# Kernel optimization log

Measured on AMD Instinct MI355X. Metric: run time of the kernel, lower is better.

## Reference

```python
import jax, jax.numpy as jnp
import numpy as np

B = 16384

def setup_inputs() -> dict:
    key = jax.random.key(0)
    ks = jax.random.split(key, 10)
    def lin(kw, fan_in, fan_out):
        lim = 1.0 / np.sqrt(fan_in)
        k1, k2 = jax.random.split(kw)
        w = jax.random.uniform(k1, (fan_out, fan_in), jnp.float32, -lim, lim)
        b = jax.random.uniform(k2, (fan_out,), jnp.float32, -lim, lim)
        return w, b
    x = jax.random.normal(ks[0], (B, 784), dtype=jnp.float32)
    conv_w = jnp.ones((3, 3), dtype=jnp.float32)
    w1, b1 = lin(ks[1], 676, 256)
    w2, b2 = lin(ks[2], 256, 128)
    w3, b3 = lin(ks[3], 128, 64)
    w4, b4 = lin(ks[4], 64, 10)
    return {"x": x, "conv_w": conv_w, "w1": w1, "b1": b1, "w2": w2, "b2": b2,
            "w3": w3, "b3": b3, "w4": w4, "b4": b4}

def reference(x, conv_w, w1, b1, w2, b2, w3, b3, w4, b4):
    b = x.shape[0]
    img = x.reshape(b, 1, 28, 28)                      # NCHW
    kern = conv_w.reshape(1, 1, 3, 3)                   # OIHW
    conv = jax.lax.conv_general_dilated(
        img, kern, window_strides=(1, 1), padding='VALID',
        dimension_numbers=('NCHW', 'OIHW', 'NCHW'))     # [B,1,26,26]
    h = conv.reshape(b, 26 * 26)
    h1 = jax.nn.relu(h @ w1.T + b1)
    h2 = jax.nn.relu(h1 @ w2.T + b2)
    h3 = jax.nn.relu(h2 @ w3.T + b3)
    out = h3 @ w4.T + b4                                # [B,10] logits
    return out
```

## Files before the change

kernel.cpp:

```cpp
#include <hip/hip_runtime.h>
#include <hip/hip_bf16.h>

typedef __attribute__((ext_vector_type(8))) short bf16x8;
typedef __attribute__((ext_vector_type(4))) float f32x4;

__device__ __forceinline__ unsigned short f2bf(float f) {
  unsigned int u = __builtin_bit_cast(unsigned int, f);
  u += 0x7fffu + ((u >> 16) & 1u);
  return (unsigned short)(u >> 16);
}

__device__ __forceinline__ f32x4 mfma16(bf16x8 a, bf16x8 b, f32x4 c) {
  return __builtin_amdgcn_mfma_f32_16x16x32_bf16(a, b, c, 0, 0, 0);
}

__global__ void prep_weights(const float* __restrict__ w1, const float* __restrict__ w2,
                             const float* __restrict__ w3, const float* __restrict__ w4,
                             unsigned short* __restrict__ w1b, unsigned short* __restrict__ w2b,
                             unsigned short* __restrict__ w3b, unsigned short* __restrict__ w4b) {
  const int idx = blockIdx.x * blockDim.x + threadIdx.x;
  const int stride = gridDim.x * blockDim.x;
  for (int i = idx; i < 256 * 704; i += stride) {
    int o = i / 704, k = i - o * 704;
    w1b[i] = f2bf(k < 676 ? w1[o * 676 + k] : 0.f);
  }
  for (int i = idx; i < 128 * 256; i += stride) w2b[i] = f2bf(w2[i]);
  for (int i = idx; i < 64 * 128; i += stride) w3b[i] = f2bf(w3[i]);
  for (int i = idx; i < 16 * 64; i += stride) {
    int o = i >> 6, k = i & 63;
    w4b[i] = f2bf(o < 10 ? w4[o * 64 + k] : 0.f);
  }
}

#define LDS_TOTAL 145408

__global__ __launch_bounds__(512, 2) void fused_mlp(
    const float* __restrict__ x,
    const float* __restrict__ cw,
    const unsigned short* __restrict__ w1b,
    const unsigned short* __restrict__ w2b,
    const unsigned short* __restrict__ w3b,
    const unsigned short* __restrict__ w4b,
    const float* __restrict__ b1, const float* __restrict__ b2,
    const float* __restrict__ b3, const float* __restrict__ b4,
    float* __restrict__ out)
{
  extern __shared__ char lds[];
  unsigned short* hbT = (unsigned short*)(lds);
  unsigned short* w1s = (unsigned short*)(lds + 91136);
  unsigned short* h1s = (unsigned short*)(lds + 111616);
  unsigned short* w2s = (unsigned short*)(lds);
  unsigned short* h2s = (unsigned short*)(lds + 91136);
  unsigned short* w3s = (unsigned short*)(lds + 111616);
  unsigned short* h3s = (unsigned short*)(lds);
  unsigned short* w4s = (unsigned short*)(lds + 91136);

  const int tid = threadIdx.x;
  const int lane = tid & 63;
  const int lane15 = lane & 15;
  const int kg = (lane >> 4) << 3;
  const int w = tid >> 6;
  const int wr = w >> 2;
  const int wc = w & 3;
  const int row0 = blockIdx.x * 64;

  {
    const float c0 = cw[0], c1 = cw[1], c2 = cw[2];
    const float c3 = cw[3], c4 = cw[4], c5 = cw[5];
    const float c6 = cw[6], c7 = cw[7], c8 = cw[8];
    const float* xblk = x + (size_t)row0 * 784;
    for (int f = tid; f < 64 * 182; f += 512) {
      int rr = f / 182;
      int t = f - rr * 182;
      int i = t / 7;
      int jq = t - i * 7;
      int j0 = jq << 2;
      const float* xr = xblk + rr * 784 + i * 28 + j0;
      if (jq < 6) {
        float4 v00 = *(const float4*)(xr);
        float4 v01 = *(const float4*)(xr + 4);
        float4 v10 = *(const float4*)(xr + 28);
        float4 v11 = *(const float4*)(xr + 32);
        float4 v20 = *(const float4*)(xr + 56);
        float4 v21 = *(const float4*)(xr + 60);
        float r0[8] = {v00.x, v00.y, v00.z, v00.w, v01.x, v01.y, v01.z, v01.w};
        float r1[8] = {v10.x, v10.y, v10.z, v10.w, v11.x, v11.y, v11.z, v11.w};
        float r2[8] = {v20.x, v20.y, v20.z, v20.w, v21.x, v21.y, v21.z, v21.w};
        float o[4];
#pragma unroll
        for (int tt = 0; tt < 4; ++tt) {
          o[tt] = c0 * r0[tt] + c1 * r0[tt + 1] + c2 * r0[tt + 2]
                + c3 * r1[tt] + c4 * r1[tt + 1] + c5 * r1[tt + 2]
                + c6 * r2[tt] + c7 * r2[tt + 1] + c8 * r2[tt + 2];
        }
        unsigned int p0 = (unsigned)f2bf(o[0]) | ((unsigned)f2bf(o[1]) << 16);
        unsigned int p1 = (unsigned)f2bf(o[2]) | ((unsigned)f2bf(o[3]) << 16);
        unsigned int* dst = (unsigned int*)(hbT + rr * 712 + i * 26 + j0);
        dst[0] = p0;
        dst[1] = p1;
      } else {
        float4 v0 = *(const float4*)(xr);
        float4 v1 = *(const float4*)(xr + 28);
        float4 v2 = *(const float4*)(xr + 56);
        float o0 = c0 * v0.x + c1 * v0.y + c2 * v0.z
                 + c3 * v1.x + c4 * v1.y + c5 * v1.z
                 + c6 * v2.x + c7 * v2.y + c8 * v2.z;
        float o1 = c0 * v0.y + c1 * v0.z + c2 * v0.w
                 + c3 * v1.y + c4 * v1.z + c5 * v1.w
                 + c6 * v2.y + c7 * v2.z + c8 * v2.w;
        unsigned int p0 = (unsigned)f2bf(o0) | ((unsigned)f2bf(o1) << 16);
        *(unsigned int*)(hbT + rr * 712 + i * 26 + 24) = p0;
      }
    }
    for (int f = tid; f < 64 * 14; f += 512) {
      int rr = f / 14, u = f - rr * 14;
      *(unsigned int*)(hbT + rr * 712 + 676 + (u << 1)) = 0u;
    }
  }

  f32x4 acc1[2][4] = {};
  __syncthreads();

  for (int ks = 0; ks < 22; ++ks) {
    const int k0 = ks << 5;
    {
      int f = tid;
#pragma unroll
      for (int it = 0; it < 2; ++it, f += 512) {
        int o = f >> 2, part = f & 3;
        *(uint4*)(w1s + o * 40 + (part << 3)) =
            *(const uint4*)(w1b + o * 704 + k0 + (part << 3));
      }
    }
    __syncthreads();
    bf16x8 a0 = *(const bf16x8*)(hbT + (wr * 32 + lane15) * 712 + k0 + kg);
    bf16x8 a1 = *(const bf16x8*)(hbT + (wr * 32 + 16 + lane15) * 712 + k0 + kg);
    bf16x8 fb0 = *(const bf16x8*)(w1s + (wc * 64 + lane15) * 40 + kg);
    bf16x8 fb1 = *(const bf16x8*)(w1s + (wc * 64 + 16 + lane15) * 40 + kg);
    bf16x8 fb2 = *(const bf16x8*)(w1s + (wc * 64 + 32 + lane15) * 40 + kg);
    bf16x8 fb3 = *(const bf16x8*)(w1s + (wc * 64 + 48 + lane15) * 40 + kg);
    acc1[0][0] = mfma16(a0, fb0, acc1[0][0]);
    acc1[0][1] = mfma16(a0, fb1, acc1[0][1]);
    acc1[0][2] = mfma16(a0, fb2, acc1[0][2]);
    acc1[0][3] = mfma16(a0, fb3, acc1[0][3]);
    acc1[1][0] = mfma16(a1, fb0, acc1[1][0]);
    acc1[1][1] = mfma16(a1, fb1, acc1[1][1]);
    acc1[1][2] = mfma16(a1, fb2, acc1[1][2]);
    acc1[1][3] = mfma16(a1, fb3, acc1[1][3]);
    __syncthreads();
  }

  {
    const int rb = wr * 32 + ((lane >> 4) << 2);
    const int cb = wc * 64 + lane15;
#pragma unroll
    for (int n = 0; n < 4; ++n) {
      const int col = cb + n * 16;
      const float bias = b1[col];
#pragma unroll
      for (int m = 0; m < 2; ++m) {
#pragma unroll
        for (int r = 0; r < 4; ++r) {
          float v = acc1[m][n][r] + bias;
          v = v > 0.f ? v : 0.f;
          h1s[(rb + m * 16 + r) * 264 + col] = f2bf(v);
        }
      }
    }
  }
  {
    int f = tid;
#pragma unroll
    for (int it = 0; it < 8; ++it, f += 512) {
      int o = f >> 5, part = f & 31;
      *(uint4*)(w2s + o * 264 + (part << 3)) =
          *(const uint4*)(w2b + o * 256 + (part << 3));
    }
  }
  __syncthreads();

  f32x4 acc2[2][2] = {};
  {
    const int ar = wr * 32 + lane15;
    const int bc = wc * 32 + lane15;
#pragma unroll
    for (int ks = 0; ks < 8; ++ks) {
      const int k0 = ks << 5;
      bf16x8 a0 = *(const bf16x8*)(h1s + ar * 264 + k0 + kg);
      bf16x8 a1 = *(const bf16x8*)(h1s + (ar + 16) * 264 + k0 + kg);
      bf16x8 fb0 = *(const bf16x8*)(w2s + bc * 264 + k0 + kg);
      bf16x8 fb1 = *(const bf16x8*)(w2s + (bc + 16) * 264 + k0 + kg);
      acc2[0][0] = mfma16(a0, fb0, acc2[0][0]);
      acc2[0][1] = mfma16(a0, fb1, acc2[0][1]);
      acc2[1][0] = mfma16(a1, fb0, acc2[1][0]);
      acc2[1][1] = mfma16(a1, fb1, acc2[1][1]);
    }
  }
  {
    const int rb = wr * 32 + ((lane >> 4) << 2);
    const int cb2 = wc * 32 + lane15;
#pragma unroll
    for (int n = 0; n < 2; ++n) {
      const int col = cb2 + n * 16;
      const float bias = b2[col];
#pragma unroll
      for (int m = 0; m < 2; ++m) {
#pragma unroll
        for (int r = 0; r < 4; ++r) {
          float v = acc2[m][n][r] + bias;
          v = v > 0.f ? v : 0.f;
          h2s[(rb + m * 16 + r) * 136 + col] = f2bf(v);
        }
      }
    }
  }
  __syncthreads();
  {
    int f = tid;
#pragma unroll
    for (int it = 0; it < 2; ++it, f += 512) {
      int o = f >> 4, part = f & 15;
      *(uint4*)(w3s + o * 136 + (part << 3)) =
          *(const uint4*)(w3b + o * 128 + (part << 3));
    }
  }
  __syncthreads();

  f32x4 acc3[2] = {};
  {
    const int ar = wr * 32 + lane15;
    const int bc3 = wc * 16 + lane15;
#pragma unroll
    for (int ks = 0; ks < 4; ++ks) {
      const int k0 = ks << 5;
      bf16x8 a0 = *(const bf16x8*)(h2s + ar * 136 + k0 + kg);
      bf16x8 a1 = *(const bf16x8*)(h2s + (ar + 16) * 136 + k0 + kg);
      bf16x8 fb0 = *(const bf16x8*)(w3s + bc3 * 136 + k0 + kg);
      acc3[0] = mfma16(a0, fb0, acc3[0]);
      acc3[1] = mfma16(a1, fb0, acc3[1]);
    }
    const int rb = wr * 32 + ((lane >> 4) << 2);
    const int col = bc3;
    const float bias = b3[col];
#pragma unroll
    for (int m = 0; m < 2; ++m) {
#pragma unroll
      for (int r = 0; r < 4; ++r) {
        float v = acc3[m][r] + bias;
        v = v > 0.f ? v : 0.f;
        h3s[(rb + m * 16 + r) * 72 + col] = f2bf(v);
      }
    }
  }
  __syncthreads();
  if (tid < 128) {
    int o = tid >> 3, part = tid & 7;
    *(uint4*)(w4s + o * 72 + (part << 3)) =
        *(const uint4*)(w4b + o * 64 + (part << 3));
  }
  __syncthreads();

  if (w < 4) {
    f32x4 acc4 = {};
    const int ar4 = w * 16 + lane15;
#pragma unroll
    for (int ks = 0; ks < 2; ++ks) {
      const int k0 = ks << 5;
      bf16x8 a0 = *(const bf16x8*)(h3s + ar4 * 72 + k0 + kg);
      bf16x8 fb0 = *(const bf16x8*)(w4s + lane15 * 72 + k0 + kg);
      acc4 = mfma16(a0, fb0, acc4);
    }
    const int col = lane15;
    if (col < 10) {
      const float bias = b4[col];
      const int rb4 = w * 16 + ((lane >> 4) << 2);
#pragma unroll
      for (int r = 0; r < 4; ++r) {
        out[(row0 + rb4 + r) * 10 + col] = acc4[r] + bias;
      }
    }
  }
}

extern "C" void kernel_launch(void* const* d_in, const int* in_sizes, int n_in,
                              void* d_out, int out_size, void* d_ws, size_t ws_size,
                              hipStream_t stream) {
  const float* x  = (const float*)d_in[0];
  const float* cw = (const float*)d_in[1];
  const float* w1 = (const float*)d_in[2];
  const float* b1 = (const float*)d_in[3];
  const float* w2 = (const float*)d_in[4];
  const float* b2 = (const float*)d_in[5];
  const float* w3 = (const float*)d_in[6];
  const float* b3 = (const float*)d_in[7];
  const float* w4 = (const float*)d_in[8];
  const float* b4 = (const float*)d_in[9];
  float* out = (float*)d_out;

  unsigned short* w1b = (unsigned short*)d_ws;
  unsigned short* w2b = w1b + 256 * 704;
  unsigned short* w3b = w2b + 128 * 256;
  unsigned short* w4b = w3b + 64 * 128;

  hipLaunchKernelGGL(prep_weights, dim3(128), dim3(256), 0, stream,
                     w1, w2, w3, w4, w1b, w2b, w3b, w4b);

  hipFuncSetAttribute((const void*)fused_mlp,
                      hipFuncAttributeMaxDynamicSharedMemorySize, LDS_TOTAL);
  hipLaunchKernelGGL(fused_mlp, dim3(256), dim3(512), LDS_TOTAL, stream,
                     x, cw, w1b, w2b, w3b, w4b, b1, b2, b3, b4, out);
}
```

Baseline: 134.6 us.

## Read weights directly from global memory and halve rows per block

Weight fragments are now loaded straight from global/L2 into MFMA operands instead of being staged through LDS with two barriers per K step. The block shrinks to 32 rows and 256 threads, with 512 blocks and about 45KB of static LDS instead of 145KB dynamic, so more blocks can fit per CU. Each wave now covers all 32 rows and a 64-column slice of layer 1. Every block rereads the full weight matrices from cache and the weight loads are uncoalesced strided row reads, which could raise L2 traffic.

New measurement: 140.3 us. 4.2% more time.

```diff
diff --git a/kernel.cpp b/kernel.cpp
--- a/kernel.cpp
+++ b/kernel.cpp
@@ -32,9 +32,7 @@
   }
 }
 
-#define LDS_TOTAL 145408
-
-__global__ __launch_bounds__(512, 2) void fused_mlp(
+__global__ __launch_bounds__(256, 2) void fused_mlp(
     const float* __restrict__ x,
     const float* __restrict__ cw,
     const unsigned short* __restrict__ w1b,
@@ -45,31 +43,26 @@
     const float* __restrict__ b3, const float* __restrict__ b4,
     float* __restrict__ out)
 {
-  extern __shared__ char lds[];
-  unsigned short* hbT = (unsigned short*)(lds);
-  unsigned short* w1s = (unsigned short*)(lds + 91136);
-  unsigned short* h1s = (unsigned short*)(lds + 111616);
-  unsigned short* w2s = (unsigned short*)(lds);
-  unsigned short* h2s = (unsigned short*)(lds + 91136);
-  unsigned short* w3s = (unsigned short*)(lds + 111616);
-  unsigned short* h3s = (unsigned short*)(lds);
-  unsigned short* w4s = (unsigned short*)(lds + 91136);
+  __shared__ unsigned short lds_s[22784];
+  unsigned short* hbT = lds_s;
+  unsigned short* h1s = lds_s;
+  unsigned short* h2s = lds_s + 8448;
+  unsigned short* h3s = lds_s + 12800;
 
   const int tid = threadIdx.x;
   const int lane = tid & 63;
   const int lane15 = lane & 15;
   const int kg = (lane >> 4) << 3;
   const int w = tid >> 6;
-  const int wr = w >> 2;
-  const int wc = w & 3;
-  const int row0 = blockIdx.x * 64;
+  const int row0 = blockIdx.x * 32;
+  const int rb = (lane >> 4) << 2;
 
   {
     const float c0 = cw[0], c1 = cw[1], c2 = cw[2];
     const float c3 = cw[3], c4 = cw[4], c5 = cw[5];
     const float c6 = cw[6], c7 = cw[7], c8 = cw[8];
     const float* xblk = x + (size_t)row0 * 784;
-    for (int f = tid; f < 64 * 182; f += 512) {
+    for (int f = tid; f < 32 * 182; f += 256) {
       int rr = f / 182;
       int t = f - rr * 182;
       int i = t / 7;
@@ -112,135 +105,108 @@
         *(unsigned int*)(hbT + rr * 712 + i * 26 + 24) = p0;
       }
     }
-    for (int f = tid; f < 64 * 14; f += 512) {
+    for (int f = tid; f < 32 * 14; f += 256) {
       int rr = f / 14, u = f - rr * 14;
       *(unsigned int*)(hbT + rr * 712 + 676 + (u << 1)) = 0u;
     }
   }
 
+  __syncthreads();
+
   f32x4 acc1[2][4] = {};
-  __syncthreads();
-
-  for (int ks = 0; ks < 22; ++ks) {
-    const int k0 = ks << 5;
-    {
-      int f = tid;
-#pragma unroll
-      for (int it = 0; it < 2; ++it, f += 512) {
-        int o = f >> 2, part = f & 3;
-        *(uint4*)(w1s + o * 40 + (part << 3)) =
-            *(const uint4*)(w1b + o * 704 + k0 + (part << 3));
-      }
-    }
-    __syncthreads();
-    bf16x8 a0 = *(const bf16x8*)(hbT + (wr * 32 + lane15) * 712 + k0 + kg);
-    bf16x8 a1 = *(const bf16x8*)(hbT + (wr * 32 + 16 + lane15) * 712 + k0 + kg);
-    bf16x8 fb0 = *(const bf16x8*)(w1s + (wc * 64 + lane15) * 40 + kg);
-    bf16x8 fb1 = *(const bf16x8*)(w1s + (wc * 64 + 16 + lane15) * 40 + kg);
-    bf16x8 fb2 = *(const bf16x8*)(w1s + (wc * 64 + 32 + lane15) * 40 + kg);
-    bf16x8 fb3 = *(const bf16x8*)(w1s + (wc * 64 + 48 + lane15) * 40 + kg);
-    acc1[0][0] = mfma16(a0, fb0, acc1[0][0]);
-    acc1[0][1] = mfma16(a0, fb1, acc1[0][1]);
-    acc1[0][2] = mfma16(a0, fb2, acc1[0][2]);
-    acc1[0][3] = mfma16(a0, fb3, acc1[0][3]);
-    acc1[1][0] = mfma16(a1, fb0, acc1[1][0]);
-    acc1[1][1] = mfma16(a1, fb1, acc1[1][1]);
-    acc1[1][2] = mfma16(a1, fb2, acc1[1][2]);
-    acc1[1][3] = mfma16(a1, fb3, acc1[1][3]);
-    __syncthreads();
-  }
-
-  {
-    const int rb = wr * 32 + ((lane >> 4) << 2);
-    const int cb = wc * 64 + lane15;
-#pragma unroll
-    for (int n = 0; n < 4; ++n) {
-      const int col = cb + n * 16;
-      const float bias = b1[col];
-#pragma unroll
-      for (int m = 0; m < 2; ++m) {
-#pragma unroll
-        for (int r = 0; r < 4; ++r) {
-          float v = acc1[m][n][r] + bias;
-          v = v > 0.f ? v : 0.f;
-          h1s[(rb + m * 16 + r) * 264 + col] = f2bf(v);
-        }
-      }
-    }
-  }
-  {
-    int f = tid;
-#pragma unroll
-    for (int it = 0; it < 8; ++it, f += 512) {
-      int o = f >> 5, part = f & 31;
-      *(uint4*)(w2s + o * 264 + (part << 3)) =
-          *(const uint4*)(w2b + o * 256 + (part << 3));
+  {
+    const unsigned short* a0p = hbT + lane15 * 712 + kg;
+    const unsigned short* a1p = hbT + (16 + lane15) * 712 + kg;
+    const unsigned short* bp = w1b + (w * 64 + lane15) * 704 + kg;
+#pragma unroll 2
+    for (int ks = 0; ks < 22; ++ks) {
+      const int k0 = ks << 5;
+      bf16x8 a0 = *(const bf16x8*)(a0p + k0);
+      bf16x8 a1 = *(const bf16x8*)(a1p + k0);
+      bf16x8 fb0 = *(const bf16x8*)(bp + k0);
+      bf16x8 fb1 = *(const bf16x8*)(bp + 16 * 704 + k0);
+      bf16x8 fb2 = *(const bf16x8*)(bp + 32 * 704 + k0);
+      bf16x8 fb3 = *(const bf16x8*)(bp + 48 * 704 + k0);
+      acc1[0][0] = mfma16(a0, fb0, acc1[0][0]);
+      acc1[1][0] = mfma16(a1, fb0, acc1[1][0]);
+      acc1[0][1] = mfma16(a0, fb1, acc1[0][1]);
+      acc1[1][1] = mfma16(a1, fb1, acc1[1][1]);
+      acc1[0][2] = mfma16(a0, fb2, acc1[0][2]);
+      acc1[1][2] = mfma16(a1, fb2, acc1[1][2]);
+      acc1[0][3] = mfma16(a0, fb3, acc1[0][3]);
+      acc1[1][3] = mfma16(a1, fb3, acc1[1][3]);
+    }
+  }
+
+  __syncthreads();
+
+#pragma unroll
+  for (int n = 0; n < 4; ++n) {
+    const int col = w * 64 + n * 16 + lane15;
+    const float bias = b1[col];
+#pragma unroll
+    for (int m = 0; m < 2; ++m) {
+#pragma unroll
+      for (int r = 0; r < 4; ++r) {
+        float v = acc1[m][n][r] + bias;
+        v = v > 0.f ? v : 0.f;
+        h1s[(rb + m * 16 + r) * 264 + col] = f2bf(v);
+      }
     }
   }
   __syncthreads();
 
   f32x4 acc2[2][2] = {};
   {
-    const int ar = wr * 32 + lane15;
-    const int bc = wc * 32 + lane15;
+    const unsigned short* a0p = h1s + lane15 * 264 + kg;
+    const unsigned short* a1p = h1s + (16 + lane15) * 264 + kg;
+    const unsigned short* bp = w2b + (w * 32 + lane15) * 256 + kg;
 #pragma unroll
     for (int ks = 0; ks < 8; ++ks) {
       const int k0 = ks << 5;
-      bf16x8 a0 = *(const bf16x8*)(h1s + ar * 264 + k0 + kg);
-      bf16x8 a1 = *(const bf16x8*)(h1s + (ar + 16) * 264 + k0 + kg);
-      bf16x8 fb0 = *(const bf16x8*)(w2s + bc * 264 + k0 + kg);
-      bf16x8 fb1 = *(const bf16x8*)(w2s + (bc + 16) * 264 + k0 + kg);
+      bf16x8 a0 = *(const bf16x8*)(a0p + k0);
+      bf16x8 a1 = *(const bf16x8*)(a1p + k0);
+      bf16x8 fb0 = *(const bf16x8*)(bp + k0);
+      bf16x8 fb1 = *(const bf16x8*)(bp + 16 * 256 + k0);
       acc2[0][0] = mfma16(a0, fb0, acc2[0][0]);
+      acc2[1][0] = mfma16(a1, fb0, acc2[1][0]);
       acc2[0][1] = mfma16(a0, fb1, acc2[0][1]);
-      acc2[1][0] = mfma16(a1, fb0, acc2[1][0]);
       acc2[1][1] = mfma16(a1, fb1, acc2[1][1]);
     }
   }
-  {
-    const int rb = wr * 32 + ((lane >> 4) << 2);
-    const int cb2 = wc * 32 + lane15;
-#pragma unroll
-    for (int n = 0; n < 2; ++n) {
-      const int col = cb2 + n * 16;
-      const float bias = b2[col];
-#pragma unroll
-      for (int m = 0; m < 2; ++m) {
-#pragma unroll
-        for (int r = 0; r < 4; ++r) {
-          float v = acc2[m][n][r] + bias;
-          v = v > 0.f ? v : 0.f;
-          h2s[(rb + m * 16 + r) * 136 + col] = f2bf(v);
-        }
-      }
-    }
-  }
-  __syncthreads();
-  {
-    int f = tid;
-#pragma unroll
-    for (int it = 0; it < 2; ++it, f += 512) {
-      int o = f >> 4, part = f & 15;
-      *(uint4*)(w3s + o * 136 + (part << 3)) =
-          *(const uint4*)(w3b + o * 128 + (part << 3));
+#pragma unroll
+  for (int n = 0; n < 2; ++n) {
+    const int col = w * 32 + n * 16 + lane15;
+    const float bias = b2[col];
+#pragma unroll
+    for (int m = 0; m < 2; ++m) {
+#pragma unroll
+      for (int r = 0; r < 4; ++r) {
+        float v = acc2[m][n][r] + bias;
+        v = v > 0.f ? v : 0.f;
+        h2s[(rb + m * 16 + r) * 136 + col] = f2bf(v);
+      }
     }
   }
   __syncthreads();
 
   f32x4 acc3[2] = {};
   {
-    const int ar = wr * 32 + lane15;
-    const int bc3 = wc * 16 + lane15;
+    const unsigned short* a0p = h2s + lane15 * 136 + kg;
+    const unsigned short* a1p = h2s + (16 + lane15) * 136 + kg;
+    const unsigned short* bp = w3b + (w * 16 + lane15) * 128 + kg;
 #pragma unroll
     for (int ks = 0; ks < 4; ++ks) {
       const int k0 = ks << 5;
-      bf16x8 a0 = *(const bf16x8*)(h2s + ar * 136 + k0 + kg);
-      bf16x8 a1 = *(const bf16x8*)(h2s + (ar + 16) * 136 + k0 + kg);
-      bf16x8 fb0 = *(const bf16x8*)(w3s + bc3 * 136 + k0 + kg);
+      bf16x8 a0 = *(const bf16x8*)(a0p + k0);
+      bf16x8 a1 = *(const bf16x8*)(a1p + k0);
+      bf16x8 fb0 = *(const bf16x8*)(bp + k0);
       acc3[0] = mfma16(a0, fb0, acc3[0]);
       acc3[1] = mfma16(a1, fb0, acc3[1]);
     }
-    const int rb = wr * 32 + ((lane >> 4) << 2);
-    const int col = bc3;
+  }
+  {
+    const int col = w * 16 + lane15;
     const float bias = b3[col];
 #pragma unroll
     for (int m = 0; m < 2; ++m) {
@@ -253,30 +219,24 @@
     }
   }
   __syncthreads();
-  if (tid < 128) {
-    int o = tid >> 3, part = tid & 7;
-    *(uint4*)(w4s + o * 72 + (part << 3)) =
-        *(const uint4*)(w4b + o * 64 + (part << 3));
-  }
-  __syncthreads();
-
-  if (w < 4) {
+
+  if (w < 2) {
     f32x4 acc4 = {};
-    const int ar4 = w * 16 + lane15;
+    const unsigned short* ap = h3s + (w * 16 + lane15) * 72 + kg;
+    const unsigned short* bp = w4b + lane15 * 64 + kg;
 #pragma unroll
     for (int ks = 0; ks < 2; ++ks) {
       const int k0 = ks << 5;
-      bf16x8 a0 = *(const bf16x8*)(h3s + ar4 * 72 + k0 + kg);
-      bf16x8 fb0 = *(const bf16x8*)(w4s + lane15 * 72 + k0 + kg);
+      bf16x8 a0 = *(const bf16x8*)(ap + k0);
+      bf16x8 fb0 = *(const bf16x8*)(bp + k0);
       acc4 = mfma16(a0, fb0, acc4);
     }
     const int col = lane15;
     if (col < 10) {
       const float bias = b4[col];
-      const int rb4 = w * 16 + ((lane >> 4) << 2);
-#pragma unroll
-      for (int r = 0; r < 4; ++r) {
-        out[(row0 + rb4 + r) * 10 + col] = acc4[r] + bias;
+#pragma unroll
+      for (int r = 0; r < 4; ++r) {
+        out[(size_t)(row0 + w * 16 + rb + r) * 10 + col] = acc4[r] + bias;
       }
     }
   }
@@ -302,11 +262,9 @@
   unsigned short* w3b = w2b + 128 * 256;
   unsigned short* w4b = w3b + 64 * 128;
 
-  hipLaunchKernelGGL(prep_weights, dim3(128), dim3(256), 0, stream,
+  hipLaunchKernelGGL(prep_weights, dim3(256), dim3(256), 0, stream,
                      w1, w2, w3, w4, w1b, w2b, w3b, w4b);
 
-  hipFuncSetAttribute((const void*)fused_mlp,
-                      hipFuncAttributeMaxDynamicSharedMemorySize, LDS_TOTAL);
-  hipLaunchKernelGGL(fused_mlp, dim3(256), dim3(512), LDS_TOTAL, stream,
+  hipLaunchKernelGGL(fused_mlp, dim3(512), dim3(256), 0, stream,
                      x, cw, w1b, w2b, w3b, w4b, b1, b2, b3, b4, out);
 }
```
